# Performance work log

Measured on AMD Instinct MI355X. Metric: run time of the kernel, lower is better.

## Reference

```python
import jax, jax.numpy as jnp
import numpy as np

DEPTH = 3
HIDDEN = 300
ATOM_FDIM = 133
BOND_FDIM = 147


def setup_inputs() -> dict:
    key = jax.random.key(0)
    ks = jax.random.split(key, 10)
    n_atoms, n_bonds, max_nb, n_mols = 200000, 400000, 6, 10000
    f_atoms = jax.random.normal(ks[0], (n_atoms, ATOM_FDIM), dtype=jnp.float32)
    f_bonds = jax.random.normal(ks[1], (n_bonds, BOND_FDIM), dtype=jnp.float32)
    a2b = jax.random.randint(ks[2], (n_atoms, max_nb), 0, n_bonds)
    b2a = jax.random.randint(ks[3], (n_bonds,), 0, n_atoms)
    b2revb = jax.random.randint(ks[4], (n_bonds,), 0, n_bonds)
    # learned parameters (fan-in scaled)
    W_i = jax.random.normal(ks[5], (BOND_FDIM, HIDDEN), dtype=jnp.float32) / np.sqrt(BOND_FDIM)
    W_h = jax.random.normal(ks[6], (HIDDEN, HIDDEN), dtype=jnp.float32) / np.sqrt(HIDDEN)
    W_o = jax.random.normal(ks[7], (ATOM_FDIM + HIDDEN, HIDDEN), dtype=jnp.float32) / np.sqrt(ATOM_FDIM + HIDDEN)
    b_o = jnp.zeros((HIDDEN,), dtype=jnp.float32)
    return {"f_atoms": f_atoms, "f_bonds": f_bonds, "a2b": a2b, "b2a": b2a,
            "b2revb": b2revb, "W_i": W_i, "W_h": W_h, "W_o": W_o, "b_o": b_o,
            "n_mols": n_mols}


def reference(f_atoms, f_bonds, a2b, b2a, b2revb, W_i, W_h, W_o, b_o, n_mols):
    act = jax.nn.relu
    # input = W_i(f_bonds); message = act(input)
    inp = f_bonds @ W_i                       # [n_bonds, H]
    message = act(inp)
    for _ in range(DEPTH - 1):
        nei_a_message = message[a2b]          # [n_atoms, max_nb, H] gather
        a_message = nei_a_message.sum(axis=1)  # [n_atoms, H]
        rev_message = message[b2revb]         # [n_bonds, H]
        message = a_message[b2a] - rev_message
        message = act(inp + message @ W_h)
    # final atom readout
    a_message = message[a2b].sum(axis=1)      # [n_atoms, H]
    a_input = jnp.concatenate([f_atoms, a_message], axis=1)
    atom_hiddens = act(a_input @ W_o + b_o)   # [n_atoms, H]
    # scope-based mean pooling (uniform molecules: n_atoms = n_mols * apm)
    apm = f_atoms.shape[0] // n_mols
    mol_vecs = atom_hiddens.reshape(n_mols, apm, HIDDEN).mean(axis=1)
    return mol_vecs
```

## Files before the change

kernel.cpp:

```cpp
#include <hip/hip_runtime.h>
#include <hip/hip_bf16.h>
#include <cstdint>
#include <cstddef>

#define HP 320

typedef unsigned short ushortT;
typedef __attribute__((ext_vector_type(8))) __bf16 bf16x8;
typedef __attribute__((ext_vector_type(4))) float f32x4;

__device__ __forceinline__ float b2f(unsigned u) {
    union { unsigned i; float f; } v; v.i = u << 16; return v.f;
}
__device__ __forceinline__ ushortT f2b(float f) {
    union { float f; unsigned i; } v; v.f = f;
    unsigned x = v.i;
    return (ushortT)((x + 0x7fffu + ((x >> 16) & 1u)) >> 16);
}
__device__ __forceinline__ unsigned subpk(unsigned a, unsigned r) {
    union { unsigned i; float f; } al, ah, rl, rh;
    al.i = a << 16; ah.i = a & 0xffff0000u;
    rl.i = r << 16; rh.i = r & 0xffff0000u;
    float lo = al.f - rl.f, hi = ah.f - rh.f;
    return (unsigned)f2b(lo) | ((unsigned)f2b(hi) << 16);
}
__device__ __forceinline__ uint4 subpk4(uint4 a, uint4 r) {
    uint4 o;
    o.x = subpk(a.x, r.x); o.y = subpk(a.y, r.y);
    o.z = subpk(a.z, r.z); o.w = subpk(a.w, r.w);
    return o;
}

__device__ __forceinline__ void pack_one(int idx, const float* __restrict__ W,
                                         int Ksrc, ushortT* __restrict__ dst) {
    int j = idx & 7, col = (idx >> 3) & 15, kg = (idx >> 7) & 3;
    int t = idx >> 9; int nt = t % 20, kt = t / 20;
    int k = kt * 32 + kg * 8 + j, n = nt * 16 + col;
    float v = (k < Ksrc && n < 300) ? W[k * 300 + n] : 0.f;
    dst[idx] = f2b(v);
}
__device__ __forceinline__ void pack_wo(int idx, const float* __restrict__ W,
                                        ushortT* __restrict__ dst) {
    int j = idx & 7, col = (idx >> 3) & 15, kg = (idx >> 7) & 3;
    int t = idx >> 9; int nt = t % 20, kt = t / 20;
    int k = kt * 32 + kg * 8 + j, n = nt * 16 + col;
    int src = (k < 133) ? k : ((k >= 160 && k < 460) ? (k - 27) : -1);
    float v = (src >= 0 && n < 300) ? W[src * 300 + n] : 0.f;
    dst[idx] = f2b(v);
}

__global__ __launch_bounds__(256) void k_pack_weights(
    const float* __restrict__ Wi, const float* __restrict__ Wh,
    const float* __restrict__ Wo, const float* __restrict__ bo,
    ushortT* __restrict__ Wipk, ushortT* __restrict__ Whpk,
    ushortT* __restrict__ Wopk, float* __restrict__ bop) {
    int idx = blockIdx.x * 256 + threadIdx.x;
    if (idx < 51200)  pack_one(idx, Wi, 147, Wipk);
    if (idx < 102400) pack_one(idx, Wh, 300, Whpk);
    if (idx < 153600) pack_wo(idx, Wo, Wopk);
    if (idx < HP) bop[idx] = (idx < 300) ? bo[idx] : 0.f;
}

template <int FD>
__global__ __launch_bounds__(256) void k_pack_feat(
    const float* __restrict__ src, ushortT* __restrict__ dst, int nrows) {
    int t = blockIdx.x * 256 + threadIdx.x;
    if (t >= nrows * 20) return;
    int row = t / 20, q = t - row * 20;
    int k0 = q * 8;
    union { ushortT u[8]; uint4 v; } o;
#pragma unroll
    for (int j = 0; j < 8; j++) {
        int k = k0 + j;
        o.u[j] = (k < FD) ? f2b(src[(size_t)row * FD + k]) : (ushortT)0;
    }
    *(uint4*)(dst + (size_t)row * 160 + k0) = o.v;
}

template <int MODE, bool AUXP>
__global__ __launch_bounds__(256, 3) void k_mfma(
    const float* __restrict__ fa, const float* __restrict__ fb,
    const ushortT* __restrict__ aux,
    const ushortT* __restrict__ amsg, const ushortT* __restrict__ msgin,
    const int* __restrict__ b2a, const int* __restrict__ b2revb,
    const ushortT* __restrict__ Bpk1, const ushortT* __restrict__ Bpk2,
    const float* __restrict__ bop,
    ushortT* __restrict__ outp) {
    constexpr int KT = (MODE == 0) ? 5 : 15;
    constexpr int SPLIT = (MODE == 1) ? 10 : KT;
    constexpr int SP = (MODE == 0) ? 168 : ((MODE == 1) ? 328 : 488);
    __shared__ __align__(16) ushortT panel[64 * SP];

    const int tid = threadIdx.x, wave = tid >> 6, lane = tid & 63;
    const int row0 = blockIdx.x * 64;
    const int kg8 = (lane >> 4) * 8;
    const int l15 = lane & 15;

    if (MODE == 1) {
#pragma unroll
        for (int it = 0; it < 10; it++) {
            int flat = tid + 256 * it;
            int row = flat / 40, ch = flat - row * 40;
            size_t oa = (size_t)b2a[row0 + row] * HP;
            size_t orv = (size_t)b2revb[row0 + row] * HP;
            uint4 ua = *(const uint4*)(amsg + oa + ch * 8);
            uint4 ur = *(const uint4*)(msgin + orv + ch * 8);
            *(uint4*)&panel[row * SP + ch * 8] = subpk4(ua, ur);
        }
    } else if (MODE == 0) {
#pragma unroll
        for (int it = 0; it < 5; it++) {
            int flat = tid + 256 * it;
            int row = flat / 20, ch = flat - row * 20;
            uint4 v;
            if (AUXP) {
                v = *(const uint4*)(aux + (size_t)(row0 + row) * 160 + ch * 8);
            } else {
                union { ushortT u[8]; uint4 w; } t;
#pragma unroll
                for (int j = 0; j < 8; j++) {
                    int k = ch * 8 + j;
                    t.u[j] = (k < 147) ? f2b(fb[(size_t)(row0 + row) * 147 + k]) : (ushortT)0;
                }
                v = t.w;
            }
            *(uint4*)&panel[row * SP + ch * 8] = v;
        }
    } else {
#pragma unroll
        for (int it = 0; it < 15; it++) {
            int flat = tid + 256 * it;
            int row = flat / 60, ch = flat - row * 60;
            uint4 v;
            if (ch >= 20) {
                v = *(const uint4*)(amsg + (size_t)(row0 + row) * HP + (ch - 20) * 8);
            } else if (AUXP) {
                v = *(const uint4*)(aux + (size_t)(row0 + row) * 160 + ch * 8);
            } else {
                union { ushortT u[8]; uint4 w; } t;
#pragma unroll
                for (int j = 0; j < 8; j++) {
                    int k = ch * 8 + j;
                    t.u[j] = (k < 133) ? f2b(fa[(size_t)(row0 + row) * 133 + k]) : (ushortT)0;
                }
                v = t.w;
            }
            *(uint4*)&panel[row * SP + ch * 8] = v;
        }
    }

    f32x4 acc[4][5];
#pragma unroll
    for (int i = 0; i < 4; i++)
#pragma unroll
        for (int n = 0; n < 5; n++) acc[i][n] = (f32x4){0.f, 0.f, 0.f, 0.f};

    uint4 breg[2][5];
    const int boff = wave * 5 * 512 + (lane >> 4) * 128 + l15 * 8;

#define LOADB(kt, buf)                                                               \
    {                                                                                \
        const ushortT* bp = ((kt) < SPLIT) ? (Bpk1 + (size_t)(kt) * 10240)           \
                                           : (Bpk2 + (size_t)((kt) - SPLIT) * 10240);\
        _Pragma("unroll")                                                            \
        for (int n = 0; n < 5; n++)                                                  \
            breg[buf][n] = *(const uint4*)(bp + boff + n * 512);                     \
    }

#define MSTEP(bufi, pk0)                                                             \
    {                                                                                \
        bf16x8 a0 = *(bf16x8*)&panel[(l15) * SP + (pk0) + kg8];                      \
        bf16x8 a1 = *(bf16x8*)&panel[(16 + l15) * SP + (pk0) + kg8];                 \
        bf16x8 a2 = *(bf16x8*)&panel[(32 + l15) * SP + (pk0) + kg8];                 \
        bf16x8 a3 = *(bf16x8*)&panel[(48 + l15) * SP + (pk0) + kg8];                 \
        __builtin_amdgcn_s_setprio(1);                                               \
        _Pragma("unroll")                                                            \
        for (int n = 0; n < 5; n++) {                                                \
            bf16x8 b;                                                                \
            *(uint4*)&b = breg[bufi][n];                                             \
            acc[0][n] = __builtin_amdgcn_mfma_f32_16x16x32_bf16(b, a0, acc[0][n], 0, 0, 0); \
            acc[1][n] = __builtin_amdgcn_mfma_f32_16x16x32_bf16(b, a1, acc[1][n], 0, 0, 0); \
            acc[2][n] = __builtin_amdgcn_mfma_f32_16x16x32_bf16(b, a2, acc[2][n], 0, 0, 0); \
            acc[3][n] = __builtin_amdgcn_mfma_f32_16x16x32_bf16(b, a3, acc[3][n], 0, 0, 0); \
        }                                                                            \
        __builtin_amdgcn_s_setprio(0);                                               \
    }

    LOADB(0, 0);
    __syncthreads();

    if (MODE == 1) {
#pragma unroll
        for (int kt = 0; kt < 10; kt++) {
            LOADB(kt + 1, (kt + 1) & 1);
            MSTEP(kt & 1, kt * 32);
        }
        __syncthreads();
#pragma unroll
        for (int it = 0; it < 5; it++) {
            int flat = tid + 256 * it;
            int row = flat / 20, ch = flat - row * 20;
            uint4 v;
            if (AUXP) {
                v = *(const uint4*)(aux + (size_t)(row0 + row) * 160 + ch * 8);
            } else {
                union { ushortT u[8]; uint4 w; } t;
#pragma unroll
                for (int j = 0; j < 8; j++) {
                    int k = ch * 8 + j;
                    t.u[j] = (k < 147) ? f2b(fb[(size_t)(row0 + row) * 147 + k]) : (ushortT)0;
                }
                v = t.w;
            }
            *(uint4*)&panel[row * SP + ch * 8] = v;
        }
        __syncthreads();
#pragma unroll
        for (int kt = 10; kt < 15; kt++) {
            if (kt + 1 < 15) LOADB(kt + 1, (kt + 1) & 1);
            MSTEP(kt & 1, (kt - 10) * 32);
        }
    } else {
#pragma unroll
        for (int kt = 0; kt < KT; kt++) {
            if (kt + 1 < KT) LOADB(kt + 1, (kt + 1) & 1);
            MSTEP(kt & 1, kt * 32);
        }
    }
#undef LOADB
#undef MSTEP

#pragma unroll
    for (int i = 0; i < 4; i++) {
        size_t gr = (size_t)(row0 + i * 16 + l15);
#pragma unroll
        for (int n = 0; n < 5; n++) {
            int col = wave * 80 + n * 16 + (lane >> 4) * 4;
            float4 v = make_float4(acc[i][n][0], acc[i][n][1], acc[i][n][2], acc[i][n][3]);
            if (MODE == 2) {
                float4 bias = *(const float4*)&bop[col];
                v.x += bias.x; v.y += bias.y; v.z += bias.z; v.w += bias.w;
            }
            ushort4 u;
            u.x = f2b(fmaxf(v.x, 0.f)); u.y = f2b(fmaxf(v.y, 0.f));
            u.z = f2b(fmaxf(v.z, 0.f)); u.w = f2b(fmaxf(v.w, 0.f));
            *(ushort4*)&outp[gr * HP + col] = u;
        }
    }
}

__global__ __launch_bounds__(256) void k_atom_sum(
    const ushortT* __restrict__ msg, const int* __restrict__ a2b,
    ushortT* __restrict__ amsg, int nA) {
    int t = blockIdx.x * 256 + threadIdx.x;
    int a = t / 40, q = t - a * 40;
    if (a >= nA) return;
    float s[8];
#pragma unroll
    for (int e = 0; e < 8; e++) s[e] = 0.f;
#pragma unroll
    for (int j = 0; j < 6; j++) {
        int b = a2b[a * 6 + j];
        uint4 u = *(const uint4*)(msg + (size_t)b * HP + q * 8);
        s[0] += b2f(u.x & 0xffff); s[1] += b2f(u.x >> 16);
        s[2] += b2f(u.y & 0xffff); s[3] += b2f(u.y >> 16);
        s[4] += b2f(u.z & 0xffff); s[5] += b2f(u.z >> 16);
        s[6] += b2f(u.w & 0xffff); s[7] += b2f(u.w >> 16);
    }
    uint4 o;
    o.x = (unsigned)f2b(s[0]) | ((unsigned)f2b(s[1]) << 16);
    o.y = (unsigned)f2b(s[2]) | ((unsigned)f2b(s[3]) << 16);
    o.z = (unsigned)f2b(s[4]) | ((unsigned)f2b(s[5]) << 16);
    o.w = (unsigned)f2b(s[6]) | ((unsigned)f2b(s[7]) << 16);
    *(uint4*)(amsg + (size_t)a * HP + q * 8) = o;
}

__global__ __launch_bounds__(256) void k_pool(
    const ushortT* __restrict__ ah, float* __restrict__ out, int n_mols, int apm) {
    int t = blockIdx.x * 256 + threadIdx.x;
    int m = t / 75, c4 = t - m * 75;
    if (m >= n_mols) return;
    float4 s = make_float4(0, 0, 0, 0);
    for (int u = 0; u < apm; u++) {
        ushort4 q = *(const ushort4*)&ah[(size_t)(m * apm + u) * HP + c4 * 4];
        s.x += b2f(q.x); s.y += b2f(q.y); s.z += b2f(q.z); s.w += b2f(q.w);
    }
    float inv = 1.0f / (float)apm;
    s.x *= inv; s.y *= inv; s.z *= inv; s.w *= inv;
    *(float4*)&out[(size_t)m * 300 + c4 * 4] = s;
}

extern "C" void kernel_launch(void* const* d_in, const int* in_sizes, int n_in,
                              void* d_out, int out_size, void* d_ws, size_t ws_size,
                              hipStream_t stream) {
    const float* fa     = (const float*)d_in[0];
    const float* fb     = (const float*)d_in[1];
    const int*   a2b    = (const int*)d_in[2];
    const int*   b2a    = (const int*)d_in[3];
    const int*   b2revb = (const int*)d_in[4];
    const float* Wi     = (const float*)d_in[5];
    const float* Wh     = (const float*)d_in[6];
    const float* Wo     = (const float*)d_in[7];
    const float* bo     = (const float*)d_in[8];

    const int nA     = in_sizes[0] / 133;
    const int nB     = in_sizes[1] / 147;
    const int n_mols = out_size / 300;
    const int apm    = nA / n_mols;

    char* p = (char*)d_ws;
    ushortT* Wipk = (ushortT*)p;  p += (size_t)51200 * 2;
    ushortT* Whpk = (ushortT*)p;  p += (size_t)102400 * 2;
    ushortT* Wopk = (ushortT*)p;  p += (size_t)153600 * 2;
    float*   bop  = (float*)p;    p += (size_t)HP * 4;
    p = (char*)(((uintptr_t)p + 255) & ~(uintptr_t)255);

    const size_t msgBytes  = (size_t)nB * HP * 2;
    const size_t amsgBytes = (size_t)nA * HP * 2;
    const size_t fbbBytes  = (size_t)nB * 160 * 2;
    const size_t faaBytes  = (size_t)nA * 160 * 2;
    const size_t headBytes = (size_t)(p - (char*)d_ws);
    const size_t baseNeed  = headBytes + 2 * msgBytes + amsgBytes;
    const bool use_fbb = ws_size >= baseNeed + fbbBytes;
    const bool use_faa = ws_size >= baseNeed + fbbBytes + faaBytes;

    ushortT* msgA = (ushortT*)p;  p += msgBytes;
    ushortT* msgB = (ushortT*)p;  p += msgBytes;
    ushortT* amsg = (ushortT*)p;  p += amsgBytes;
    ushortT* fbb  = use_fbb ? (ushortT*)p : nullptr;  p += use_fbb ? fbbBytes : 0;
    ushortT* faa  = use_faa ? (ushortT*)p : nullptr;
    ushortT* ah   = msgB;
    float*   out  = (float*)d_out;

    k_pack_weights<<<600, 256, 0, stream>>>(Wi, Wh, Wo, bo, Wipk, Whpk, Wopk, bop);
    if (use_fbb)
        k_pack_feat<147><<<(nB * 20 + 255) / 256, 256, 0, stream>>>(fb, fbb, nB);
    if (use_faa)
        k_pack_feat<133><<<(nA * 20 + 255) / 256, 256, 0, stream>>>(fa, faa, nA);

    const int asum_grid = (int)(((size_t)nA * 40 + 255) / 256);
    const int gB = nB / 64, gA = nA / 64;

    if (use_fbb)
        k_mfma<0, true ><<<gB, 256, 0, stream>>>(fa, fb, fbb, nullptr, nullptr, nullptr, nullptr,
                                                 Wipk, Wipk, bop, msgA);
    else
        k_mfma<0, false><<<gB, 256, 0, stream>>>(fa, fb, nullptr, nullptr, nullptr, nullptr, nullptr,
                                                 Wipk, Wipk, bop, msgA);

    k_atom_sum<<<asum_grid, 256, 0, stream>>>(msgA, a2b, amsg, nA);
    if (use_fbb)
        k_mfma<1, true ><<<gB, 256, 0, stream>>>(fa, fb, fbb, amsg, msgA, b2a, b2revb,
                                                 Whpk, Wipk, bop, msgB);
    else
        k_mfma<1, false><<<gB, 256, 0, stream>>>(fa, fb, nullptr, amsg, msgA, b2a, b2revb,
                                                 Whpk, Wipk, bop, msgB);

    k_atom_sum<<<asum_grid, 256, 0, stream>>>(msgB, a2b, amsg, nA);
    if (use_fbb)
        k_mfma<1, true ><<<gB, 256, 0, stream>>>(fa, fb, fbb, amsg, msgB, b2a, b2revb,
                                                 Whpk, Wipk, bop, msgA);
    else
        k_mfma<1, false><<<gB, 256, 0, stream>>>(fa, fb, nullptr, amsg, msgB, b2a, b2revb,
                                                 Whpk, Wipk, bop, msgA);

    k_atom_sum<<<asum_grid, 256, 0, stream>>>(msgA, a2b, amsg, nA);
    if (use_faa)
        k_mfma<2, true ><<<gA, 256, 0, stream>>>(fa, fb, faa, amsg, nullptr, nullptr, nullptr,
                                                 Wopk, Wopk, bop, ah);
    else
        k_mfma<2, false><<<gA, 256, 0, stream>>>(fa, fb, nullptr, amsg, nullptr, nullptr, nullptr,
                                                 Wopk, Wopk, bop, ah);
    k_pool<<<((n_mols * 75) + 255) / 256, 256, 0, stream>>>(ah, out, n_mols, apm);
}
```

Baseline: 1.329 ms.

## Fuse feature packing into first GEMM and atom-sum gather into readout GEMM

Removes the separate bf16 packing kernels. The first message GEMM now converts f_bonds itself and writes the packed copy for later layers, and the readout GEMM converts f_atoms on the fly. The final atom-sum kernel is folded into the readout kernel, which gathers and sums the six neighbour messages per atom while loading its LDS panel. The gather indices are staged in shared memory. This saves several launches and the amsg round trip, at the cost of more irregular gather work inside the GEMM's load phase.

```diff
diff --git a/kernel.cpp b/kernel.cpp
--- a/kernel.cpp
+++ b/kernel.cpp
@@ -28,6 +28,20 @@
     uint4 o;
     o.x = subpk(a.x, r.x); o.y = subpk(a.y, r.y);
     o.z = subpk(a.z, r.z); o.w = subpk(a.w, r.w);
+    return o;
+}
+__device__ __forceinline__ void upadd(uint4 u, float* s) {
+    s[0] += b2f(u.x & 0xffff); s[1] += b2f(u.x >> 16);
+    s[2] += b2f(u.y & 0xffff); s[3] += b2f(u.y >> 16);
+    s[4] += b2f(u.z & 0xffff); s[5] += b2f(u.z >> 16);
+    s[6] += b2f(u.w & 0xffff); s[7] += b2f(u.w >> 16);
+}
+__device__ __forceinline__ uint4 pk8(const float* s) {
+    uint4 o;
+    o.x = (unsigned)f2b(s[0]) | ((unsigned)f2b(s[1]) << 16);
+    o.y = (unsigned)f2b(s[2]) | ((unsigned)f2b(s[3]) << 16);
+    o.z = (unsigned)f2b(s[4]) | ((unsigned)f2b(s[5]) << 16);
+    o.w = (unsigned)f2b(s[6]) | ((unsigned)f2b(s[7]) << 16);
     return o;
 }
 
@@ -61,35 +75,25 @@
     if (idx < HP) bop[idx] = (idx < 300) ? bo[idx] : 0.f;
 }
 
-template <int FD>
-__global__ __launch_bounds__(256) void k_pack_feat(
-    const float* __restrict__ src, ushortT* __restrict__ dst, int nrows) {
-    int t = blockIdx.x * 256 + threadIdx.x;
-    if (t >= nrows * 20) return;
-    int row = t / 20, q = t - row * 20;
-    int k0 = q * 8;
-    union { ushortT u[8]; uint4 v; } o;
-#pragma unroll
-    for (int j = 0; j < 8; j++) {
-        int k = k0 + j;
-        o.u[j] = (k < FD) ? f2b(src[(size_t)row * FD + k]) : (ushortT)0;
-    }
-    *(uint4*)(dst + (size_t)row * 160 + k0) = o.v;
-}
-
 template <int MODE, bool AUXP>
 __global__ __launch_bounds__(256, 3) void k_mfma(
     const float* __restrict__ fa, const float* __restrict__ fb,
     const ushortT* __restrict__ aux,
-    const ushortT* __restrict__ amsg, const ushortT* __restrict__ msgin,
+    const ushortT* __restrict__ amsg,
+    const ushortT* __restrict__ msgin,
     const int* __restrict__ b2a, const int* __restrict__ b2revb,
+    const int* __restrict__ a2b,
     const ushortT* __restrict__ Bpk1, const ushortT* __restrict__ Bpk2,
     const float* __restrict__ bop,
-    ushortT* __restrict__ outp) {
+    ushortT* __restrict__ outp,
+    ushortT* __restrict__ auxw) {
     constexpr int KT = (MODE == 0) ? 5 : 15;
     constexpr int SPLIT = (MODE == 1) ? 10 : KT;
     constexpr int SP = (MODE == 0) ? 168 : ((MODE == 1) ? 328 : 488);
     __shared__ __align__(16) ushortT panel[64 * SP];
+    __shared__ int idxA[(MODE == 1) ? 64 : 1];
+    __shared__ int idxR[(MODE == 1) ? 64 : 1];
+    __shared__ int idx6[(MODE == 2) ? 64 * 6 : 1];
 
     const int tid = threadIdx.x, wave = tid >> 6, lane = tid & 63;
     const int row0 = blockIdx.x * 64;
@@ -97,12 +101,27 @@
     const int l15 = lane & 15;
 
     if (MODE == 1) {
+        if (tid < 64) {
+            idxA[tid] = b2a[row0 + tid];
+            idxR[tid] = b2revb[row0 + tid];
+        }
+        __syncthreads();
+    } else if (MODE == 2) {
+        if (tid < 64) {
+            int a = row0 + tid;
+#pragma unroll
+            for (int j = 0; j < 6; j++) idx6[tid * 6 + j] = a2b[a * 6 + j];
+        }
+        __syncthreads();
+    }
+
+    if (MODE == 1) {
 #pragma unroll
         for (int it = 0; it < 10; it++) {
             int flat = tid + 256 * it;
             int row = flat / 40, ch = flat - row * 40;
-            size_t oa = (size_t)b2a[row0 + row] * HP;
-            size_t orv = (size_t)b2revb[row0 + row] * HP;
+            size_t oa = (size_t)idxA[row] * HP;
+            size_t orv = (size_t)idxR[row] * HP;
             uint4 ua = *(const uint4*)(amsg + oa + ch * 8);
             uint4 ur = *(const uint4*)(msgin + orv + ch * 8);
             *(uint4*)&panel[row * SP + ch * 8] = subpk4(ua, ur);
@@ -112,19 +131,14 @@
         for (int it = 0; it < 5; it++) {
             int flat = tid + 256 * it;
             int row = flat / 20, ch = flat - row * 20;
-            uint4 v;
-            if (AUXP) {
-                v = *(const uint4*)(aux + (size_t)(row0 + row) * 160 + ch * 8);
-            } else {
-                union { ushortT u[8]; uint4 w; } t;
-#pragma unroll
-                for (int j = 0; j < 8; j++) {
-                    int k = ch * 8 + j;
-                    t.u[j] = (k < 147) ? f2b(fb[(size_t)(row0 + row) * 147 + k]) : (ushortT)0;
-                }
-                v = t.w;
+            union { ushortT u[8]; uint4 w; } t;
+#pragma unroll
+            for (int j = 0; j < 8; j++) {
+                int k = ch * 8 + j;
+                t.u[j] = (k < 147) ? f2b(fb[(size_t)(row0 + row) * 147 + k]) : (ushortT)0;
             }
-            *(uint4*)&panel[row * SP + ch * 8] = v;
+            *(uint4*)&panel[row * SP + ch * 8] = t.w;
+            if (AUXP) *(uint4*)(auxw + (size_t)(row0 + row) * 160 + ch * 8) = t.w;
         }
     } else {
 #pragma unroll
@@ -133,9 +147,16 @@
             int row = flat / 60, ch = flat - row * 60;
             uint4 v;
             if (ch >= 20) {
-                v = *(const uint4*)(amsg + (size_t)(row0 + row) * HP + (ch - 20) * 8);
-            } else if (AUXP) {
-                v = *(const uint4*)(aux + (size_t)(row0 + row) * 160 + ch * 8);
+                int kc = (ch - 20) * 8;
+                float s[8];
+#pragma unroll
+                for (int e = 0; e < 8; e++) s[e] = 0.f;
+#pragma unroll
+                for (int j = 0; j < 6; j++) {
+                    uint4 u = *(const uint4*)(msgin + (size_t)idx6[row * 6 + j] * HP + kc);
+                    upadd(u, s);
+                }
+                v = pk8(s);
             } else {
                 union { ushortT u[8]; uint4 w; } t;
 #pragma unroll
@@ -262,17 +283,9 @@
     for (int j = 0; j < 6; j++) {
         int b = a2b[a * 6 + j];
         uint4 u = *(const uint4*)(msg + (size_t)b * HP + q * 8);
-        s[0] += b2f(u.x & 0xffff); s[1] += b2f(u.x >> 16);
-        s[2] += b2f(u.y & 0xffff); s[3] += b2f(u.y >> 16);
-        s[4] += b2f(u.z & 0xffff); s[5] += b2f(u.z >> 16);
-        s[6] += b2f(u.w & 0xffff); s[7] += b2f(u.w >> 16);
-    }
-    uint4 o;
-    o.x = (unsigned)f2b(s[0]) | ((unsigned)f2b(s[1]) << 16);
-    o.y = (unsigned)f2b(s[2]) | ((unsigned)f2b(s[3]) << 16);
-    o.z = (unsigned)f2b(s[4]) | ((unsigned)f2b(s[5]) << 16);
-    o.w = (unsigned)f2b(s[6]) | ((unsigned)f2b(s[7]) << 16);
-    *(uint4*)(amsg + (size_t)a * HP + q * 8) = o;
+        upadd(u, s);
+    }
+    *(uint4*)(amsg + (size_t)a * HP + q * 8) = pk8(s);
 }
 
 __global__ __launch_bounds__(256) void k_pool(
@@ -318,58 +331,45 @@
     const size_t msgBytes  = (size_t)nB * HP * 2;
     const size_t amsgBytes = (size_t)nA * HP * 2;
     const size_t fbbBytes  = (size_t)nB * 160 * 2;
-    const size_t faaBytes  = (size_t)nA * 160 * 2;
     const size_t headBytes = (size_t)(p - (char*)d_ws);
-    const size_t baseNeed  = headBytes + 2 * msgBytes + amsgBytes;
-    const bool use_fbb = ws_size >= baseNeed + fbbBytes;
-    const bool use_faa = ws_size >= baseNeed + fbbBytes + faaBytes;
+    const bool use_fbb = ws_size >= headBytes + 2 * msgBytes + amsgBytes + fbbBytes;
 
     ushortT* msgA = (ushortT*)p;  p += msgBytes;
     ushortT* msgB = (ushortT*)p;  p += msgBytes;
     ushortT* amsg = (ushortT*)p;  p += amsgBytes;
-    ushortT* fbb  = use_fbb ? (ushortT*)p : nullptr;  p += use_fbb ? fbbBytes : 0;
-    ushortT* faa  = use_faa ? (ushortT*)p : nullptr;
+    ushortT* fbb  = use_fbb ? (ushortT*)p : nullptr;
     ushortT* ah   = msgB;
     float*   out  = (float*)d_out;
 
     k_pack_weights<<<600, 256, 0, stream>>>(Wi, Wh, Wo, bo, Wipk, Whpk, Wopk, bop);
-    if (use_fbb)
-        k_pack_feat<147><<<(nB * 20 + 255) / 256, 256, 0, stream>>>(fb, fbb, nB);
-    if (use_faa)
-        k_pack_feat<133><<<(nA * 20 + 255) / 256, 256, 0, stream>>>(fa, faa, nA);
 
     const int asum_grid = (int)(((size_t)nA * 40 + 255) / 256);
     const int gB = nB / 64, gA = nA / 64;
 
     if (use_fbb)
-        k_mfma<0, true ><<<gB, 256, 0, stream>>>(fa, fb, fbb, nullptr, nullptr, nullptr, nullptr,
-                                                 Wipk, Wipk, bop, msgA);
+        k_mfma<0, true ><<<gB, 256, 0, stream>>>(fa, fb, nullptr, nullptr, nullptr, nullptr, nullptr,
+                                                 nullptr, Wipk, Wipk, bop, msgA, fbb);
     else
         k_mfma<0, false><<<gB, 256, 0, stream>>>(fa, fb, nullptr, nullptr, nullptr, nullptr, nullptr,
-                                                 Wipk, Wipk, bop, msgA);
+                                                 nullptr, Wipk, Wipk, bop, msgA, nullptr);
 
     k_atom_sum<<<asum_grid, 256, 0, stream>>>(msgA, a2b, amsg, nA);
     if (use_fbb)
-        k_mfma<1, true ><<<gB, 256, 0, stream>>>(fa, fb, fbb, amsg, msgA, b2a, b2revb,
-                                                 Whpk, Wipk, bop, msgB);
+        k_mfma<1, true ><<<gB, 256, 0, stream>>>(fa, fb, fbb, amsg, msgA, b2a, b2revb, nullptr,
+                                                 Whpk, Wipk, bop, msgB, nullptr);
     else
-        k_mfma<1, false><<<gB, 256, 0, stream>>>(fa, fb, nullptr, amsg, msgA, b2a, b2revb,
-                                                 Whpk, Wipk, bop, msgB);
+        k_mfma<1, false><<<gB, 256, 0, stream>>>(fa, fb, nullptr, amsg, msgA, b2a, b2revb, nullptr,
+                                                 Whpk, Wipk, bop, msgB, nullptr);
 
     k_atom_sum<<<asum_grid, 256, 0, stream>>>(msgB, a2b, amsg, nA);
     if (use_fbb)
-        k_mfma<1, true ><<<gB, 256, 0, stream>>>(fa, fb, fbb, amsg, msgB, b2a, b2revb,
-                                                 Whpk, Wipk, bop, msgA);
+        k_mfma<1, true ><<<gB, 256, 0, stream>>>(fa, fb, fbb, amsg, msgB, b2a, b2revb, nullptr,
+                                                 Whpk, Wipk, bop, msgA, nullptr);
     else
-        k_mfma<1, false><<<gB, 256, 0, stream>>>(fa, fb, nullptr, amsg, msgB, b2a, b2revb,
-                                                 Whpk, Wipk, bop, msgA);
-
-    k_atom_sum<<<asum_grid, 256, 0, stream>>>(msgA, a2b, amsg, nA);
-    if (use_faa)
-        k_mfma<2, true ><<<gA, 256, 0, stream>>>(fa, fb, faa, amsg, nullptr, nullptr, nullptr,
-                                                 Wopk, Wopk, bop, ah);
-    else
-        k_mfma<2, false><<<gA, 256, 0, stream>>>(fa, fb, nullptr, amsg, nullptr, nullptr, nullptr,
-                                                 Wopk, Wopk, bop, ah);
+        k_mfma<1, false><<<gB, 256, 0, stream>>>(fa, fb, nullptr, amsg, msgB, b2a, b2revb, nullptr,
+                                                 Whpk, Wipk, bop, msgA, nullptr);
+
+    k_mfma<2, false><<<gA, 256, 0, stream>>>(fa, fb, nullptr, nullptr, msgA, nullptr, nullptr, a2b,
+                                             Wopk, Wopk, bop, ah, nullptr);
     k_pool<<<((n_mols * 75) + 255) / 256, 256, 0, stream>>>(ah, out, n_mols, apm);
 }
```

After: 1.363 ms. +2.6%, slower.
